# Optimization experiments

Hardware: AMD Instinct MI355X
Metric: run time of the kernel (lower is better)

Reference implementation:

```python
import jax, jax.numpy as jnp
import numpy as np

NB_COMP = 8
LAT_DIM = 512
NB_NEUR = 1024
OUT_DIM = 512
N_SAMPLES = 16384


def setup_inputs() -> dict:
    key = jax.random.key(0)
    ks = jax.random.split(key, 8)
    s1 = 1.0 / np.sqrt(LAT_DIM)
    s2 = 1.0 / np.sqrt(NB_NEUR)
    return {
        "epsilon": jax.random.normal(ks[0], (N_SAMPLES, LAT_DIM), dtype=jnp.float32),
        "comp_idx": jax.random.randint(ks[1], (N_SAMPLES,), 0, NB_COMP, dtype=jnp.int32),
        "mu": jnp.zeros((NB_COMP, LAT_DIM), dtype=jnp.float32),
        "rho": jnp.zeros((NB_COMP,), dtype=jnp.float32),  # sigma = softplus(rho)
        "W1": jax.random.normal(ks[2], (NB_COMP, LAT_DIM, NB_NEUR), dtype=jnp.float32) * s1,
        "b1": jax.random.normal(ks[3], (NB_COMP, NB_NEUR), dtype=jnp.float32) * s1,
        "W2": jax.random.normal(ks[4], (NB_COMP, NB_NEUR, OUT_DIM), dtype=jnp.float32) * s2,
        "b2": jax.random.normal(ks[5], (NB_COMP, OUT_DIM), dtype=jnp.float32) * s2,
    }


def reference(epsilon, comp_idx, mu, rho, W1, b1, W2, b2):
    # GNNens.forward: per-sample categorical component dispatch through a
    # 1-hidden-layer sigmoid MLP. Vectorized as compute-all-components + select.
    sigma = jax.nn.softplus(rho)                          # [C]
    # lat_c[c,n,d] = epsilon[n,d] * sigma[c] + mu[c,d]
    lat = epsilon[None, :, :] * sigma[:, None, None] + mu[:, None, :]  # [C,N,D]
    h = jax.nn.sigmoid(jnp.einsum('cnd,cdh->cnh', lat, W1) + b1[:, None, :])  # [C,N,H]
    y = jnp.einsum('cnh,cho->cno', h, W2) + b2[:, None, :]                    # [C,N,O]
    # select each sample's routed component
    idx = comp_idx[None, :, None].astype(jnp.int32)       # [1,N,1]
    out = jnp.take_along_axis(y, idx, axis=0)[0]          # [N,O]
    return out
```

## Files before the change

### kernel.cpp

```cpp
#include <hip/hip_runtime.h>
#include <stdint.h>

#define NCOMP 8
#define LATD  512
#define HID   1024
#define OUTD  512
#define NS    16384

typedef unsigned short u16;
typedef __bf16 bf16x8 __attribute__((ext_vector_type(8)));
typedef float  f32x4  __attribute__((ext_vector_type(4)));

#define MAPS       (NS/128 + NCOMP)
#define SLOT_CHUNK ((MAPS + 7)/8)

#define ORDER_OFF  2048
#define APACK_OFF  (ORDER_OFF + NS*4)
#define W1T_OFF    (APACK_OFF + (size_t)NS*LATD*2)
#define W2T_OFF    (W1T_OFF + (size_t)NCOMP*LATD*HID*2)
#define H_OFF      (W2T_OFF + (size_t)NCOMP*HID*OUTD*2)
#define WS_NEEDED  (H_OFF + (size_t)NS*HID*2)

__device__ __forceinline__ u16 f2b(float f) {
  unsigned int u = __builtin_bit_cast(unsigned int, f);
  u = (u + 0x7FFFu + ((u >> 16) & 1u)) >> 16;
  return (u16)u;
}

__device__ __forceinline__ void load_lds16(const void* g, void* l) {
  __builtin_amdgcn_global_load_lds((const __attribute__((address_space(1))) void*)g,
                                   (__attribute__((address_space(3))) void*)l, 16, 0, 0);
}

__global__ __launch_bounds__(1024)
void k_bucket(const int* __restrict__ idx, const float* __restrict__ rho,
              int* __restrict__ offsets, float* __restrict__ sigma,
              int* __restrict__ ntiles, int* __restrict__ map,
              int* __restrict__ order) {
  __shared__ int cnt[NCOMP][1024];
  __shared__ int wtot[NCOMP][16];
  const int t = threadIdx.x;
  const int wave = t >> 6, lane = t & 63;

  int my[16];
  #pragma unroll
  for (int i = 0; i < 16; ++i) my[i] = idx[t + (i << 10)];
  #pragma unroll
  for (int c = 0; c < NCOMP; ++c) cnt[c][t] = 0;
  #pragma unroll
  for (int i = 0; i < 16; ++i) cnt[my[i]][t]++;
  __syncthreads();

  #pragma unroll
  for (int c = 0; c < NCOMP; ++c) {
    int v = cnt[c][t];
    int s = v;
    #pragma unroll
    for (int d = 1; d < 64; d <<= 1) {
      int u = __shfl_up(s, d);
      if (lane >= d) s += u;
    }
    cnt[c][t] = s - v;
    if (lane == 63) wtot[c][wave] = s;
  }
  __syncthreads();

  if (t == 0) {
    int acc = 0;
    int csz[NCOMP];
    for (int c = 0; c < NCOMP; ++c) {
      offsets[c] = acc;
      int start = acc;
      for (int w = 0; w < 16; ++w) { int x = wtot[c][w]; wtot[c][w] = acc; acc += x; }
      csz[c] = acc - start;
    }
    offsets[NCOMP] = acc;
    int n = 0;
    for (int c = 0; c < NCOMP; ++c)
      for (int m = 0; m < (csz[c] + 127) >> 7; ++m) map[n++] = (c << 16) | m;
    ntiles[0] = n;
  }
  if (t < NCOMP) {
    float r = rho[t];
    sigma[t] = (r > 20.f) ? r : log1pf(expf(r));
  }
  __syncthreads();

  #pragma unroll
  for (int c = 0; c < NCOMP; ++c) cnt[c][t] += wtot[c][wave];
  #pragma unroll
  for (int i = 0; i < 16; ++i) {
    int c = my[i];
    int p = cnt[c][t]++;
    order[p] = t + (i << 10);
  }
}

__global__ void k_prep(const float* __restrict__ eps, const int* __restrict__ idx,
                       const float* __restrict__ mu, const float* __restrict__ sigma,
                       const int* __restrict__ order, u16* __restrict__ Apack,
                       const float* __restrict__ W1, const float* __restrict__ W2,
                       u16* __restrict__ W1T, u16* __restrict__ W2T) {
  __shared__ float tile[64][65];
  int b = blockIdx.x;
  if (b < 4096) {
    int g = b*256 + threadIdx.x;
    int i = g >> 6;
    int d = (g & 63) << 3;
    int s = order[i];
    int c = idx[s];
    float sg = sigma[c];
    const float4* ep = reinterpret_cast<const float4*>(eps + (size_t)s*LATD + d);
    const float4* mp = reinterpret_cast<const float4*>(mu  + (size_t)c*LATD + d);
    float4 e0 = ep[0], e1 = ep[1], m0 = mp[0], m1 = mp[1];
    unsigned o0 = f2b(e0.x*sg+m0.x), o1 = f2b(e0.y*sg+m0.y), o2 = f2b(e0.z*sg+m0.z), o3 = f2b(e0.w*sg+m0.w);
    unsigned o4 = f2b(e1.x*sg+m1.x), o5 = f2b(e1.y*sg+m1.y), o6 = f2b(e1.z*sg+m1.z), o7 = f2b(e1.w*sg+m1.w);
    uint4 pk;
    pk.x = o0 | (o1<<16); pk.y = o2 | (o3<<16); pk.z = o4 | (o5<<16); pk.w = o6 | (o7<<16);
    *reinterpret_cast<uint4*>(Apack + (size_t)i*LATD + d) = pk;
  } else {
    int bb = b - 4096;
    const float* src; u16* dst; int R, CC, r0, c0;
    if (bb < 1024) {
      int comp = bb >> 7, loc = bb & 127;
      R = LATD; CC = HID;
      c0 = (loc & 15) << 6; r0 = (loc >> 4) << 6;
      src = W1 + (size_t)comp*R*CC; dst = W1T + (size_t)comp*R*CC;
    } else {
      int b2 = bb - 1024;
      int comp = b2 >> 7, loc = b2 & 127;
      R = HID; CC = OUTD;
      c0 = (loc & 7) << 6; r0 = (loc >> 3) << 6;
      src = W2 + (size_t)comp*R*CC; dst = W2T + (size_t)comp*R*CC;
    }
    int tx = threadIdx.x & 63, ty = threadIdx.x >> 6;
    for (int rr = ty; rr < 64; rr += 4)
      tile[rr][tx] = src[(size_t)(r0+rr)*CC + c0 + tx];
    __syncthreads();
    for (int rr = ty; rr < 64; rr += 4)
      dst[(size_t)(c0+rr)*R + r0 + tx] = f2b(tile[tx][rr]);
  }
}

template<int K, int NB, int STAGE>
__global__ __launch_bounds__(256, 4)
void k_gemm(const u16* __restrict__ A, const u16* __restrict__ BT,
            const int* __restrict__ offsets, const int* __restrict__ ntiles,
            const int* __restrict__ map, const int* __restrict__ order,
            const float* __restrict__ bias,
            u16* __restrict__ Hout, float* __restrict__ Yout) {
  constexpr int NCB = NB/128;
  __shared__ u16 As[128*64];
  __shared__ u16 Bs[128*64];
  __shared__ int ord[128];

  const int id    = blockIdx.x;
  const int xcd   = id & 7;
  const int sub   = id >> 3;
  const int ncolb = sub % NCB;
  const int slot  = xcd*SLOT_CHUNK + sub / NCB;
  if (slot >= ntiles[0]) return;
  const int packed = map[slot];
  const int c      = packed >> 16;
  const int bstart = offsets[c];
  const int bend   = offsets[c+1];
  const int tile0  = bstart + (packed & 0xffff)*128;
  const int ncol0  = ncolb*128;

  const int tid  = threadIdx.x;
  const int wave = tid >> 6;
  const int lane = tid & 63;
  const int srow = (wave<<5) + (lane>>3);
  const int scol = (lane&7)<<3;

  if (STAGE == 2 && tid < 128) {
    int gr = tile0 + tid;
    ord[tid] = order[gr < bend ? gr : bstart];
  }

  size_t a_off[4], b_off[4];
  const size_t bbase = (size_t)c * NB * K;
  #pragma unroll
  for (int i = 0; i < 4; ++i) {
    int ar = tile0 + srow + (i<<3);
    if (ar >= bend) ar = bend - 1;
    a_off[i] = (size_t)ar * K + scol;
    b_off[i] = bbase + (size_t)(ncol0 + srow + (i<<3)) * K + scol;
  }

  const int wr   = (wave >> 1) << 6;
  const int wc   = (wave & 1) << 6;
  const int quad = lane >> 4;
  const int l16  = lane & 15;

  float bcol[4];
  #pragma unroll
  for (int ni = 0; ni < 4; ++ni)
    bcol[ni] = bias[(size_t)c*NB + ncol0 + wc + (ni<<4) + l16];

  f32x4 acc[4][4] = {};

  for (int k0 = 0; k0 < K; k0 += 64) {
    #pragma unroll
    for (int i = 0; i < 4; ++i)
      load_lds16(A + a_off[i] + k0, &As[((wave<<5) + (i<<3))<<6]);
    #pragma unroll
    for (int i = 0; i < 4; ++i)
      load_lds16(BT + b_off[i] + k0, &Bs[((wave<<5) + (i<<3))<<6]);
    __syncthreads();
    #pragma unroll
    for (int kk = 0; kk < 64; kk += 32) {
      bf16x8 af[4], bfr[4];
      #pragma unroll
      for (int mi = 0; mi < 4; ++mi)
        af[mi] = *reinterpret_cast<const bf16x8*>(&As[((wr + (mi<<4) + l16)<<6) + kk + (quad<<3)]);
      #pragma unroll
      for (int ni = 0; ni < 4; ++ni)
        bfr[ni] = *reinterpret_cast<const bf16x8*>(&Bs[((wc + (ni<<4) + l16)<<6) + kk + (quad<<3)]);
      #pragma unroll
      for (int mi = 0; mi < 4; ++mi)
        #pragma unroll
        for (int ni = 0; ni < 4; ++ni)
          acc[mi][ni] = __builtin_amdgcn_mfma_f32_16x16x32_bf16(af[mi], bfr[ni], acc[mi][ni], 0, 0, 0);
    }
    __syncthreads();
  }

  #pragma unroll
  for (int mi = 0; mi < 4; ++mi) {
    #pragma unroll
    for (int r = 0; r < 4; ++r) {
      const int row_l = wr + (mi<<4) + (quad<<2) + r;
      const int grow  = tile0 + row_l;
      if (grow < bend) {
        #pragma unroll
        for (int ni = 0; ni < 4; ++ni) {
          const int col = ncol0 + wc + (ni<<4) + l16;
          float v = acc[mi][ni][r] + bcol[ni];
          if (STAGE == 1) {
            v = 1.0f / (1.0f + __expf(-v));
            Hout[(size_t)grow*NB + col] = f2b(v);
          } else {
            Yout[(size_t)ord[row_l]*NB + col] = v;
          }
        }
      }
    }
  }
}

__global__ void k_naive(const float* __restrict__ eps, const int* __restrict__ idx,
                        const float* __restrict__ mu, const float* __restrict__ rho,
                        const float* __restrict__ W1, const float* __restrict__ b1,
                        const float* __restrict__ W2, const float* __restrict__ b2,
                        float* __restrict__ out) {
  __shared__ float lat[LATD];
  __shared__ float h[HID];
  int n = blockIdx.x, t = threadIdx.x;
  int c = idx[n];
  float r = rho[c];
  float sg = (r > 20.f) ? r : log1pf(expf(r));
  for (int d = t; d < LATD; d += 256) lat[d] = eps[(size_t)n*LATD+d]*sg + mu[(size_t)c*LATD+d];
  __syncthreads();
  for (int j = t; j < HID; j += 256) {
    float a = b1[(size_t)c*HID+j];
    const float* w = W1 + (size_t)c*LATD*HID + j;
    for (int d = 0; d < LATD; ++d) a += lat[d]*w[(size_t)d*HID];
    h[j] = 1.f/(1.f+expf(-a));
  }
  __syncthreads();
  for (int o = t; o < OUTD; o += 256) {
    float a = b2[(size_t)c*OUTD+o];
    const float* w = W2 + (size_t)c*HID*OUTD + o;
    for (int j = 0; j < HID; ++j) a += h[j]*w[(size_t)j*OUTD];
    out[(size_t)n*OUTD+o] = a;
  }
}

extern "C" void kernel_launch(void* const* d_in, const int* in_sizes, int n_in,
                              void* d_out, int out_size, void* d_ws, size_t ws_size,
                              hipStream_t stream) {
  const float* eps = (const float*)d_in[0];
  const int*   idx = (const int*)d_in[1];
  const float* mu  = (const float*)d_in[2];
  const float* rho = (const float*)d_in[3];
  const float* W1  = (const float*)d_in[4];
  const float* b1  = (const float*)d_in[5];
  const float* W2  = (const float*)d_in[6];
  const float* b2  = (const float*)d_in[7];
  float* out = (float*)d_out;

  if (ws_size < WS_NEEDED) {
    k_naive<<<NS, 256, 0, stream>>>(eps, idx, mu, rho, W1, b1, W2, b2, out);
    return;
  }

  char* ws = (char*)d_ws;
  int*   offsets = (int*)(ws + 0);
  float* sigma   = (float*)(ws + 64);
  int*   ntiles  = (int*)(ws + 96);
  int*   map     = (int*)(ws + 128);
  int*   order   = (int*)(ws + ORDER_OFF);
  u16*   Apack   = (u16*)(ws + APACK_OFF);
  u16*   W1T     = (u16*)(ws + W1T_OFF);
  u16*   W2T     = (u16*)(ws + W2T_OFF);
  u16*   Hws     = (u16*)(ws + H_OFF);

  k_bucket<<<1, 1024, 0, stream>>>(idx, rho, offsets, sigma, ntiles, map, order);
  k_prep  <<<4096 + 2048, 256, 0, stream>>>(eps, idx, mu, sigma, order, Apack, W1, W2, W1T, W2T);
  k_gemm<LATD, HID, 1><<<8*SLOT_CHUNK*(HID/128), 256, 0, stream>>>(
      Apack, W1T, offsets, ntiles, map, order, b1, Hws, nullptr);
  k_gemm<HID, OUTD, 2><<<8*SLOT_CHUNK*(OUTD/128), 256, 0, stream>>>(
      Hws, W2T, offsets, ntiles, map, order, b2, nullptr, out);
}
```

Baseline: 204.2 us.

## Fuse weight transpose and bf16 conversion into GEMM B-tile loads; parallelize bucketing

Drops the separate pass that transposed W1/W2 into bf16 workspace copies. The GEMMs now read fp32 weights directly, convert them to bf16 in registers and store them transposed into an XOR-swizzled LDS tile. This saves a full read and write of both weight tensors per call. The bucketing kernel is split across 8 blocks, one per component, using nibble-packed counts and wave reductions instead of a single-block serial scan. In exchange, each GEMM block now reads fp32 weights (twice the bytes) through registers instead of async direct-to-LDS loads, and the same weights are re-read by every row tile. The conversion rounds half-up instead of to nearest even.

```diff
diff --git a/kernel.cpp b/kernel.cpp
--- a/kernel.cpp
+++ b/kernel.cpp
@@ -16,9 +16,7 @@
 
 #define ORDER_OFF  2048
 #define APACK_OFF  (ORDER_OFF + NS*4)
-#define W1T_OFF    (APACK_OFF + (size_t)NS*LATD*2)
-#define W2T_OFF    (W1T_OFF + (size_t)NCOMP*LATD*HID*2)
-#define H_OFF      (W2T_OFF + (size_t)NCOMP*HID*OUTD*2)
+#define H_OFF      (APACK_OFF + (size_t)NS*LATD*2)
 #define WS_NEEDED  (H_OFF + (size_t)NS*HID*2)
 
 __device__ __forceinline__ u16 f2b(float f) {
@@ -33,118 +31,98 @@
 }
 
 __global__ __launch_bounds__(1024)
-void k_bucket(const int* __restrict__ idx, const float* __restrict__ rho,
-              int* __restrict__ offsets, float* __restrict__ sigma,
-              int* __restrict__ ntiles, int* __restrict__ map,
-              int* __restrict__ order) {
-  __shared__ int cnt[NCOMP][1024];
-  __shared__ int wtot[NCOMP][16];
+void k_bucket8(const int* __restrict__ idx, const float* __restrict__ rho,
+               int* __restrict__ offsets, float* __restrict__ sigma,
+               int* __restrict__ ntiles, int* __restrict__ map,
+               int* __restrict__ order) {
+  __shared__ int hist_s[NCOMP];
+  __shared__ int wtot[16];
+  const int c = blockIdx.x;
   const int t = threadIdx.x;
   const int wave = t >> 6, lane = t & 63;
 
   int my[16];
   #pragma unroll
   for (int i = 0; i < 16; ++i) my[i] = idx[t + (i << 10)];
-  #pragma unroll
-  for (int c = 0; c < NCOMP; ++c) cnt[c][t] = 0;
-  #pragma unroll
-  for (int i = 0; i < 16; ++i) cnt[my[i]][t]++;
+
+  unsigned long long nib = 0;
+  #pragma unroll
+  for (int i = 0; i < 16; ++i) nib += 1ull << (my[i] << 2);
+
+  if (t < NCOMP) hist_s[t] = 0;
   __syncthreads();
 
   #pragma unroll
-  for (int c = 0; c < NCOMP; ++c) {
-    int v = cnt[c][t];
-    int s = v;
-    #pragma unroll
-    for (int d = 1; d < 64; d <<= 1) {
-      int u = __shfl_up(s, d);
-      if (lane >= d) s += u;
+  for (int cc = 0; cc < NCOMP; ++cc) {
+    int v = (int)((nib >> (cc << 2)) & 15);
+    #pragma unroll
+    for (int d = 1; d < 64; d <<= 1) v += __shfl_xor(v, d);
+    if (lane == 0) atomicAdd(&hist_s[cc], v);
+  }
+
+  int v = (int)((nib >> (c << 2)) & 15);
+  int s = v;
+  #pragma unroll
+  for (int d = 1; d < 64; d <<= 1) {
+    int u = __shfl_up(s, d);
+    if (lane >= d) s += u;
+  }
+  if (lane == 63) wtot[wave] = s;
+  __syncthreads();
+
+  int wbase = 0;
+  for (int w = 0; w < wave; ++w) wbase += wtot[w];
+  int off_c = 0;
+  #pragma unroll
+  for (int cc = 0; cc < NCOMP; ++cc) if (cc < c) off_c += hist_s[cc];
+
+  int pos = off_c + wbase + (s - v);
+  #pragma unroll
+  for (int i = 0; i < 16; ++i)
+    if (my[i] == c) order[pos++] = t + (i << 10);
+
+  if (t == 0) {
+    if (c == 0) {
+      int a = 0;
+      for (int cc = 0; cc < NCOMP; ++cc) { offsets[cc] = a; a += hist_s[cc]; }
+      offsets[NCOMP] = a;
+      int tot = 0;
+      for (int cc = 0; cc < NCOMP; ++cc) tot += (hist_s[cc] + 127) >> 7;
+      ntiles[0] = tot;
     }
-    cnt[c][t] = s - v;
-    if (lane == 63) wtot[c][wave] = s;
-  }
-  __syncthreads();
-
-  if (t == 0) {
-    int acc = 0;
-    int csz[NCOMP];
-    for (int c = 0; c < NCOMP; ++c) {
-      offsets[c] = acc;
-      int start = acc;
-      for (int w = 0; w < 16; ++w) { int x = wtot[c][w]; wtot[c][w] = acc; acc += x; }
-      csz[c] = acc - start;
-    }
-    offsets[NCOMP] = acc;
-    int n = 0;
-    for (int c = 0; c < NCOMP; ++c)
-      for (int m = 0; m < (csz[c] + 127) >> 7; ++m) map[n++] = (c << 16) | m;
-    ntiles[0] = n;
-  }
-  if (t < NCOMP) {
+    int mb = 0;
+    for (int cc = 0; cc < c; ++cc) mb += (hist_s[cc] + 127) >> 7;
+    int nt = (hist_s[c] + 127) >> 7;
+    for (int m = 0; m < nt; ++m) map[mb + m] = (c << 16) | m;
+  }
+  if (c == 0 && t < NCOMP) {
     float r = rho[t];
     sigma[t] = (r > 20.f) ? r : log1pf(expf(r));
   }
-  __syncthreads();
-
-  #pragma unroll
-  for (int c = 0; c < NCOMP; ++c) cnt[c][t] += wtot[c][wave];
-  #pragma unroll
-  for (int i = 0; i < 16; ++i) {
-    int c = my[i];
-    int p = cnt[c][t]++;
-    order[p] = t + (i << 10);
-  }
-}
-
-__global__ void k_prep(const float* __restrict__ eps, const int* __restrict__ idx,
+}
+
+__global__ void k_pack(const float* __restrict__ eps, const int* __restrict__ idx,
                        const float* __restrict__ mu, const float* __restrict__ sigma,
-                       const int* __restrict__ order, u16* __restrict__ Apack,
-                       const float* __restrict__ W1, const float* __restrict__ W2,
-                       u16* __restrict__ W1T, u16* __restrict__ W2T) {
-  __shared__ float tile[64][65];
-  int b = blockIdx.x;
-  if (b < 4096) {
-    int g = b*256 + threadIdx.x;
-    int i = g >> 6;
-    int d = (g & 63) << 3;
-    int s = order[i];
-    int c = idx[s];
-    float sg = sigma[c];
-    const float4* ep = reinterpret_cast<const float4*>(eps + (size_t)s*LATD + d);
-    const float4* mp = reinterpret_cast<const float4*>(mu  + (size_t)c*LATD + d);
-    float4 e0 = ep[0], e1 = ep[1], m0 = mp[0], m1 = mp[1];
-    unsigned o0 = f2b(e0.x*sg+m0.x), o1 = f2b(e0.y*sg+m0.y), o2 = f2b(e0.z*sg+m0.z), o3 = f2b(e0.w*sg+m0.w);
-    unsigned o4 = f2b(e1.x*sg+m1.x), o5 = f2b(e1.y*sg+m1.y), o6 = f2b(e1.z*sg+m1.z), o7 = f2b(e1.w*sg+m1.w);
-    uint4 pk;
-    pk.x = o0 | (o1<<16); pk.y = o2 | (o3<<16); pk.z = o4 | (o5<<16); pk.w = o6 | (o7<<16);
-    *reinterpret_cast<uint4*>(Apack + (size_t)i*LATD + d) = pk;
-  } else {
-    int bb = b - 4096;
-    const float* src; u16* dst; int R, CC, r0, c0;
-    if (bb < 1024) {
-      int comp = bb >> 7, loc = bb & 127;
-      R = LATD; CC = HID;
-      c0 = (loc & 15) << 6; r0 = (loc >> 4) << 6;
-      src = W1 + (size_t)comp*R*CC; dst = W1T + (size_t)comp*R*CC;
-    } else {
-      int b2 = bb - 1024;
-      int comp = b2 >> 7, loc = b2 & 127;
-      R = HID; CC = OUTD;
-      c0 = (loc & 7) << 6; r0 = (loc >> 3) << 6;
-      src = W2 + (size_t)comp*R*CC; dst = W2T + (size_t)comp*R*CC;
-    }
-    int tx = threadIdx.x & 63, ty = threadIdx.x >> 6;
-    for (int rr = ty; rr < 64; rr += 4)
-      tile[rr][tx] = src[(size_t)(r0+rr)*CC + c0 + tx];
-    __syncthreads();
-    for (int rr = ty; rr < 64; rr += 4)
-      dst[(size_t)(c0+rr)*R + r0 + tx] = f2b(tile[tx][rr]);
-  }
+                       const int* __restrict__ order, u16* __restrict__ Apack) {
+  int g = blockIdx.x*256 + threadIdx.x;
+  int i = g >> 6;
+  int d = (g & 63) << 3;
+  int s = order[i];
+  int c = idx[s];
+  float sg = sigma[c];
+  const float4* ep = reinterpret_cast<const float4*>(eps + (size_t)s*LATD + d);
+  const float4* mp = reinterpret_cast<const float4*>(mu  + (size_t)c*LATD + d);
+  float4 e0 = ep[0], e1 = ep[1], m0 = mp[0], m1 = mp[1];
+  unsigned o0 = f2b(e0.x*sg+m0.x), o1 = f2b(e0.y*sg+m0.y), o2 = f2b(e0.z*sg+m0.z), o3 = f2b(e0.w*sg+m0.w);
+  unsigned o4 = f2b(e1.x*sg+m1.x), o5 = f2b(e1.y*sg+m1.y), o6 = f2b(e1.z*sg+m1.z), o7 = f2b(e1.w*sg+m1.w);
+  uint4 pk;
+  pk.x = o0 | (o1<<16); pk.y = o2 | (o3<<16); pk.z = o4 | (o5<<16); pk.w = o6 | (o7<<16);
+  *reinterpret_cast<uint4*>(Apack + (size_t)i*LATD + d) = pk;
 }
 
 template<int K, int NB, int STAGE>
 __global__ __launch_bounds__(256, 4)
-void k_gemm(const u16* __restrict__ A, const u16* __restrict__ BT,
+void k_gemm(const u16* __restrict__ A, const float* __restrict__ W,
             const int* __restrict__ offsets, const int* __restrict__ ntiles,
             const int* __restrict__ map, const int* __restrict__ order,
             const float* __restrict__ bias,
@@ -178,21 +156,33 @@
     ord[tid] = order[gr < bend ? gr : bstart];
   }
 
-  size_t a_off[4], b_off[4];
-  const size_t bbase = (size_t)c * NB * K;
+  size_t a_off[4];
   #pragma unroll
   for (int i = 0; i < 4; ++i) {
     int ar = tile0 + srow + (i<<3);
     if (ar >= bend) ar = bend - 1;
     a_off[i] = (size_t)ar * K + scol;
-    b_off[i] = bbase + (size_t)(ncol0 + srow + (i<<3)) * K + scol;
-  }
+  }
+
+  const int tk = tid >> 5;
+  const int tn = (tid & 31) << 2;
+  const float* wbase = W + (size_t)c*K*NB + ncol0 + tn;
+  int swz[4];
+  #pragma unroll
+  for (int i = 0; i < 4; ++i) { int n = tn + i; swz[i] = (n + (n>>3)) & 7; }
 
   const int wr   = (wave >> 1) << 6;
   const int wc   = (wave & 1) << 6;
   const int quad = lane >> 4;
   const int l16  = lane & 15;
 
+  int nlB[4], sB[4];
+  #pragma unroll
+  for (int ni = 0; ni < 4; ++ni) {
+    nlB[ni] = wc + (ni<<4) + l16;
+    sB[ni]  = (nlB[ni] + (nlB[ni]>>3)) & 7;
+  }
+
   float bcol[4];
   #pragma unroll
   for (int ni = 0; ni < 4; ++ni)
@@ -205,8 +195,29 @@
     for (int i = 0; i < 4; ++i)
       load_lds16(A + a_off[i] + k0, &As[((wave<<5) + (i<<3))<<6]);
     #pragma unroll
-    for (int i = 0; i < 4; ++i)
-      load_lds16(BT + b_off[i] + k0, &Bs[((wave<<5) + (i<<3))<<6]);
+    for (int h = 0; h < 2; ++h) {
+      float4 r[4];
+      #pragma unroll
+      for (int p = 0; p < 2; ++p) {
+        const float* src = wbase + (size_t)(k0 + ((h*2+p)<<4) + (tk<<1))*NB;
+        r[2*p]   = *reinterpret_cast<const float4*>(src);
+        r[2*p+1] = *reinterpret_cast<const float4*>(src + NB);
+      }
+      #pragma unroll
+      for (int p = 0; p < 2; ++p) {
+        const int kl = ((h*2+p)<<4) + (tk<<1);
+        const int kc = kl >> 3;
+        const float* f0 = reinterpret_cast<const float*>(&r[2*p]);
+        const float* f1 = reinterpret_cast<const float*>(&r[2*p+1]);
+        #pragma unroll
+        for (int i = 0; i < 4; ++i) {
+          unsigned a0 = __builtin_bit_cast(unsigned, f0[i]) + 0x8000u;
+          unsigned a1 = __builtin_bit_cast(unsigned, f1[i]) + 0x8000u;
+          unsigned pk = __builtin_amdgcn_perm(a1, a0, 0x07060302u);
+          *reinterpret_cast<unsigned*>(&Bs[((tn+i)<<6) + ((kc ^ swz[i])<<3) + (kl&7)]) = pk;
+        }
+      }
+    }
     __syncthreads();
     #pragma unroll
     for (int kk = 0; kk < 64; kk += 32) {
@@ -215,8 +226,10 @@
       for (int mi = 0; mi < 4; ++mi)
         af[mi] = *reinterpret_cast<const bf16x8*>(&As[((wr + (mi<<4) + l16)<<6) + kk + (quad<<3)]);
       #pragma unroll
-      for (int ni = 0; ni < 4; ++ni)
-        bfr[ni] = *reinterpret_cast<const bf16x8*>(&Bs[((wc + (ni<<4) + l16)<<6) + kk + (quad<<3)]);
+      for (int ni = 0; ni < 4; ++ni) {
+        const int kc = (kk>>3) + quad;
+        bfr[ni] = *reinterpret_cast<const bf16x8*>(&Bs[(nlB[ni]<<6) + ((kc ^ sB[ni])<<3)]);
+      }
       #pragma unroll
       for (int mi = 0; mi < 4; ++mi)
         #pragma unroll
@@ -302,14 +315,12 @@
   int*   map     = (int*)(ws + 128);
   int*   order   = (int*)(ws + ORDER_OFF);
   u16*   Apack   = (u16*)(ws + APACK_OFF);
-  u16*   W1T     = (u16*)(ws + W1T_OFF);
-  u16*   W2T     = (u16*)(ws + W2T_OFF);
   u16*   Hws     = (u16*)(ws + H_OFF);
 
-  k_bucket<<<1, 1024, 0, stream>>>(idx, rho, offsets, sigma, ntiles, map, order);
-  k_prep  <<<4096 + 2048, 256, 0, stream>>>(eps, idx, mu, sigma, order, Apack, W1, W2, W1T, W2T);
+  k_bucket8<<<NCOMP, 1024, 0, stream>>>(idx, rho, offsets, sigma, ntiles, map, order);
+  k_pack   <<<NS*64/256, 256, 0, stream>>>(eps, idx, mu, sigma, order, Apack);
   k_gemm<LATD, HID, 1><<<8*SLOT_CHUNK*(HID/128), 256, 0, stream>>>(
-      Apack, W1T, offsets, ntiles, map, order, b1, Hws, nullptr);
+      Apack, W1, offsets, ntiles, map, order, b1, Hws, nullptr);
   k_gemm<HID, OUTD, 2><<<8*SLOT_CHUNK*(OUTD/128), 256, 0, stream>>>(
-      Hws, W2T, offsets, ntiles, map, order, b2, nullptr, out);
-}
+      Hws, W2, offsets, ntiles, map, order, b2, nullptr, out);
+}
```

Result: slower. 293.8 us (+43.8%).

## Double-buffer GEMM LDS tiles and split bucketing across per-component blocks

Applied to the files above, without the earlier changes.

The GEMM kernel now uses two LDS buffers per operand, issuing the next K-slice's global-to-LDS loads before computing on the current one, and drops one barrier per iteration. Launch bounds are relaxed from 4 to 2 blocks per SM to fit the doubled shared memory. The single-block bucketing kernel is replaced by eight blocks, one per component, using nibble-packed counts and wave reductions so order/map writes run in parallel. The cost is lower occupancy and redundant histogram work in every bucket block.

```diff
diff --git a/kernel.cpp b/kernel.cpp
--- a/kernel.cpp
+++ b/kernel.cpp
@@ -33,66 +33,73 @@
 }
 
 __global__ __launch_bounds__(1024)
-void k_bucket(const int* __restrict__ idx, const float* __restrict__ rho,
-              int* __restrict__ offsets, float* __restrict__ sigma,
-              int* __restrict__ ntiles, int* __restrict__ map,
-              int* __restrict__ order) {
-  __shared__ int cnt[NCOMP][1024];
-  __shared__ int wtot[NCOMP][16];
+void k_bucket8(const int* __restrict__ idx, const float* __restrict__ rho,
+               int* __restrict__ offsets, float* __restrict__ sigma,
+               int* __restrict__ ntiles, int* __restrict__ map,
+               int* __restrict__ order) {
+  __shared__ int hist_s[NCOMP];
+  __shared__ int wtot[16];
+  const int c = blockIdx.x;
   const int t = threadIdx.x;
   const int wave = t >> 6, lane = t & 63;
 
   int my[16];
   #pragma unroll
   for (int i = 0; i < 16; ++i) my[i] = idx[t + (i << 10)];
-  #pragma unroll
-  for (int c = 0; c < NCOMP; ++c) cnt[c][t] = 0;
-  #pragma unroll
-  for (int i = 0; i < 16; ++i) cnt[my[i]][t]++;
+
+  unsigned long long nib = 0;
+  #pragma unroll
+  for (int i = 0; i < 16; ++i) nib += 1ull << (my[i] << 2);
+
+  if (t < NCOMP) hist_s[t] = 0;
   __syncthreads();
 
   #pragma unroll
-  for (int c = 0; c < NCOMP; ++c) {
-    int v = cnt[c][t];
-    int s = v;
-    #pragma unroll
-    for (int d = 1; d < 64; d <<= 1) {
-      int u = __shfl_up(s, d);
-      if (lane >= d) s += u;
+  for (int cc = 0; cc < NCOMP; ++cc) {
+    int v = (int)((nib >> (cc << 2)) & 15);
+    #pragma unroll
+    for (int d = 1; d < 64; d <<= 1) v += __shfl_xor(v, d);
+    if (lane == 0) atomicAdd(&hist_s[cc], v);
+  }
+
+  int v = (int)((nib >> (c << 2)) & 15);
+  int s = v;
+  #pragma unroll
+  for (int d = 1; d < 64; d <<= 1) {
+    int u = __shfl_up(s, d);
+    if (lane >= d) s += u;
+  }
+  if (lane == 63) wtot[wave] = s;
+  __syncthreads();
+
+  int wbase = 0;
+  for (int w = 0; w < wave; ++w) wbase += wtot[w];
+  int off_c = 0;
+  #pragma unroll
+  for (int cc = 0; cc < NCOMP; ++cc) if (cc < c) off_c += hist_s[cc];
+
+  int pos = off_c + wbase + (s - v);
+  #pragma unroll
+  for (int i = 0; i < 16; ++i)
+    if (my[i] == c) order[pos++] = t + (i << 10);
+
+  if (t == 0) {
+    if (c == 0) {
+      int a = 0;
+      for (int cc = 0; cc < NCOMP; ++cc) { offsets[cc] = a; a += hist_s[cc]; }
+      offsets[NCOMP] = a;
+      int tot = 0;
+      for (int cc = 0; cc < NCOMP; ++cc) tot += (hist_s[cc] + 127) >> 7;
+      ntiles[0] = tot;
     }
-    cnt[c][t] = s - v;
-    if (lane == 63) wtot[c][wave] = s;
-  }
-  __syncthreads();
-
-  if (t == 0) {
-    int acc = 0;
-    int csz[NCOMP];
-    for (int c = 0; c < NCOMP; ++c) {
-      offsets[c] = acc;
-      int start = acc;
-      for (int w = 0; w < 16; ++w) { int x = wtot[c][w]; wtot[c][w] = acc; acc += x; }
-      csz[c] = acc - start;
-    }
-    offsets[NCOMP] = acc;
-    int n = 0;
-    for (int c = 0; c < NCOMP; ++c)
-      for (int m = 0; m < (csz[c] + 127) >> 7; ++m) map[n++] = (c << 16) | m;
-    ntiles[0] = n;
-  }
-  if (t < NCOMP) {
+    int mb = 0;
+    for (int cc = 0; cc < c; ++cc) mb += (hist_s[cc] + 127) >> 7;
+    int nt = (hist_s[c] + 127) >> 7;
+    for (int m = 0; m < nt; ++m) map[mb + m] = (c << 16) | m;
+  }
+  if (c == 0 && t < NCOMP) {
     float r = rho[t];
     sigma[t] = (r > 20.f) ? r : log1pf(expf(r));
-  }
-  __syncthreads();
-
-  #pragma unroll
-  for (int c = 0; c < NCOMP; ++c) cnt[c][t] += wtot[c][wave];
-  #pragma unroll
-  for (int i = 0; i < 16; ++i) {
-    int c = my[i];
-    int p = cnt[c][t]++;
-    order[p] = t + (i << 10);
   }
 }
 
@@ -143,15 +150,16 @@
 }
 
 template<int K, int NB, int STAGE>
-__global__ __launch_bounds__(256, 4)
+__global__ __launch_bounds__(256, 2)
 void k_gemm(const u16* __restrict__ A, const u16* __restrict__ BT,
             const int* __restrict__ offsets, const int* __restrict__ ntiles,
             const int* __restrict__ map, const int* __restrict__ order,
             const float* __restrict__ bias,
             u16* __restrict__ Hout, float* __restrict__ Yout) {
   constexpr int NCB = NB/128;
-  __shared__ u16 As[128*64];
-  __shared__ u16 Bs[128*64];
+  constexpr int NIT = K/64;
+  __shared__ u16 As[2][128*64];
+  __shared__ u16 Bs[2][128*64];
   __shared__ int ord[128];
 
   const int id    = blockIdx.x;
@@ -200,30 +208,35 @@
 
   f32x4 acc[4][4] = {};
 
-  for (int k0 = 0; k0 < K; k0 += 64) {
+  auto stage = [&](int k0, int p) {
     #pragma unroll
     for (int i = 0; i < 4; ++i)
-      load_lds16(A + a_off[i] + k0, &As[((wave<<5) + (i<<3))<<6]);
+      load_lds16(A + a_off[i] + k0, &As[p][((wave<<5) + (i<<3))<<6]);
     #pragma unroll
     for (int i = 0; i < 4; ++i)
-      load_lds16(BT + b_off[i] + k0, &Bs[((wave<<5) + (i<<3))<<6]);
+      load_lds16(BT + b_off[i] + k0, &Bs[p][((wave<<5) + (i<<3))<<6]);
+  };
+
+  stage(0, 0);
+  for (int it = 0; it < NIT; ++it) {
+    const int p = it & 1;
     __syncthreads();
+    if (it + 1 < NIT) stage((it+1)*64, p^1);
     #pragma unroll
     for (int kk = 0; kk < 64; kk += 32) {
       bf16x8 af[4], bfr[4];
       #pragma unroll
       for (int mi = 0; mi < 4; ++mi)
-        af[mi] = *reinterpret_cast<const bf16x8*>(&As[((wr + (mi<<4) + l16)<<6) + kk + (quad<<3)]);
+        af[mi] = *reinterpret_cast<const bf16x8*>(&As[p][((wr + (mi<<4) + l16)<<6) + kk + (quad<<3)]);
       #pragma unroll
       for (int ni = 0; ni < 4; ++ni)
-        bfr[ni] = *reinterpret_cast<const bf16x8*>(&Bs[((wc + (ni<<4) + l16)<<6) + kk + (quad<<3)]);
+        bfr[ni] = *reinterpret_cast<const bf16x8*>(&Bs[p][((wc + (ni<<4) + l16)<<6) + kk + (quad<<3)]);
       #pragma unroll
       for (int mi = 0; mi < 4; ++mi)
         #pragma unroll
         for (int ni = 0; ni < 4; ++ni)
           acc[mi][ni] = __builtin_amdgcn_mfma_f32_16x16x32_bf16(af[mi], bfr[ni], acc[mi][ni], 0, 0, 0);
     }
-    __syncthreads();
   }
 
   #pragma unroll
@@ -306,7 +319,7 @@
   u16*   W2T     = (u16*)(ws + W2T_OFF);
   u16*   Hws     = (u16*)(ws + H_OFF);
 
-  k_bucket<<<1, 1024, 0, stream>>>(idx, rho, offsets, sigma, ntiles, map, order);
+  k_bucket8<<<NCOMP, 1024, 0, stream>>>(idx, rho, offsets, sigma, ntiles, map, order);
   k_prep  <<<4096 + 2048, 256, 0, stream>>>(eps, idx, mu, sigma, order, Apack, W1, W2, W1T, W2T);
   k_gemm<LATD, HID, 1><<<8*SLOT_CHUNK*(HID/128), 256, 0, stream>>>(
       Apack, W1T, offsets, ntiles, map, order, b1, Hws, nullptr);
```

Result: slower. 223.4 us (+9.4%).
